# Performance work log

Hardware: AMD Instinct MI355X
Metric: run time of the kernel (lower is better)

Reference implementation:

```python
import jax, jax.numpy as jnp
import numpy as np

T = 524288
D = 256
N = 8192

def setup_inputs() -> dict:
    key = jax.random.key(0)
    k1, k2, k3 = jax.random.split(key, 3)
    embedding = jax.random.normal(k1, (T, D), dtype=jnp.float32)
    W = jax.random.normal(k2, (D, D), dtype=jnp.float32) * (1.0 / np.sqrt(D))
    obj_to_img = jnp.sort(jax.random.randint(k3, (T,), 0, N))
    return {"embedding": embedding, "W": W, "obj_to_img": obj_to_img, "num_segments": N}

def reference(embedding, W, obj_to_img, num_segments):
    # Per-segment mean of embedding @ W  -> global context [N, D]
    proj = embedding @ W  # [T, D]
    seg_sum = jax.ops.segment_sum(proj, obj_to_img, num_segments=num_segments)  # [N, D]
    counts = jax.ops.segment_sum(jnp.ones((embedding.shape[0],), embedding.dtype),
                                 obj_to_img, num_segments=num_segments)  # [N]
    safe_counts = jnp.maximum(counts, 1.0)
    transformed_global = jnp.tanh(seg_sum / safe_counts[:, None])  # [N, D]
    # sigmoid(emb . tg[segment]) per token
    scores = jax.nn.sigmoid(jnp.sum(embedding * transformed_global[obj_to_img], axis=-1))  # [T]
    # per-segment weighted sum of embeddings
    rep = jax.ops.segment_sum(embedding * scores[:, None], obj_to_img, num_segments=num_segments)  # [N, D]
    # broadcast representation back to every token of its segment (repeat_interleave)
    return rep[obj_to_img]  # [T, D]
```

## Files before the change

### kernel.cpp

```cpp
#include <hip/hip_runtime.h>
#include <math.h>

#define D 256
#define NSEG 8192

__device__ __forceinline__ int lower_bound_dev(const int* __restrict__ a, int n, int key) {
    int lo = 0, hi = n;
    while (lo < hi) {
        int mid = (lo + hi) >> 1;
        if (a[mid] < key) lo = mid + 1; else hi = mid;
    }
    return lo;
}

__global__ __launch_bounds__(256) void fused_seg_kernel(
        const float* __restrict__ emb,
        const float* __restrict__ W,
        const int*   __restrict__ obj, int T,
        float* __restrict__ out) {
    const int seg   = blockIdx.x;
    const int start = lower_bound_dev(obj, T, seg);
    const int end   = lower_bound_dev(obj, T, seg + 1);
    if (start >= end) return;

    const int tid  = threadIdx.x;
    const int lane = tid & 63;
    const int w    = tid >> 6;

    __shared__ float sm[4][D];
    __shared__ float sv[D];
    __shared__ float tg[D];

    float4 acc = make_float4(0.f, 0.f, 0.f, 0.f);
    for (int r = start + w; r < end; r += 4) {
        const float4 e = *reinterpret_cast<const float4*>(emb + (size_t)r * D + lane * 4);
        acc.x += e.x; acc.y += e.y; acc.z += e.z; acc.w += e.w;
    }
    *reinterpret_cast<float4*>(&sm[w][lane * 4]) = acc;
    __syncthreads();
    sv[tid] = sm[0][tid] + sm[1][tid] + sm[2][tid] + sm[3][tid];
    __syncthreads();

    const float inv = 1.0f / (float)(end - start);
    float p = 0.f;
    #pragma unroll 8
    for (int k = 0; k < D; ++k) {
        p += sv[k] * W[k * D + tid];
    }
    tg[tid] = tanhf(p * inv);
    __syncthreads();
    const float4 tg4 = *reinterpret_cast<const float4*>(&tg[lane * 4]);

    float4 racc = make_float4(0.f, 0.f, 0.f, 0.f);
    for (int r = start + w; r < end; r += 4) {
        const float4 e = *reinterpret_cast<const float4*>(emb + (size_t)r * D + lane * 4);
        float pd = e.x * tg4.x + e.y * tg4.y + e.z * tg4.z + e.w * tg4.w;
        #pragma unroll
        for (int off = 32; off >= 1; off >>= 1) pd += __shfl_xor(pd, off, 64);
        const float score = 1.0f / (1.0f + __expf(-pd));
        racc.x += e.x * score; racc.y += e.y * score;
        racc.z += e.z * score; racc.w += e.w * score;
    }
    *reinterpret_cast<float4*>(&sm[w][lane * 4]) = racc;
    __syncthreads();
    sm[0][tid] = sm[0][tid] + sm[1][tid] + sm[2][tid] + sm[3][tid];
    __syncthreads();
    const float4 rep4 = *reinterpret_cast<const float4*>(&sm[0][lane * 4]);

    for (int r = start + w; r < end; r += 4) {
        *reinterpret_cast<float4*>(out + (size_t)r * D + lane * 4) = rep4;
    }
}

extern "C" void kernel_launch(void* const* d_in, const int* in_sizes, int n_in,
                              void* d_out, int out_size, void* d_ws, size_t ws_size,
                              hipStream_t stream) {
    const float* emb = (const float*)d_in[0];
    const float* W   = (const float*)d_in[1];
    const int*   obj = (const int*)d_in[2];
    const int T = in_sizes[2];
    float* out = (float*)d_out;

    fused_seg_kernel<<<NSEG, 256, 0, stream>>>(emb, W, obj, T, out);
}
```

Measured before the change: 991.0 us.

## Precompute segment boundaries and process two segments per block to share W

Adds a separate kernel that writes the start index of every segment into workspace, replacing the per-block binary searches over obj_to_img. The fused kernel now handles two segments per block, so each W load feeds two projection accumulators and total W traffic is halved. In exchange it adds a second launch, serial per-segment phases with extra barriers inside each block, and half as many blocks.

```diff
diff --git a/kernel.cpp b/kernel.cpp
--- a/kernel.cpp
+++ b/kernel.cpp
@@ -3,72 +3,92 @@
 
 #define D 256
 #define NSEG 8192
+#define G 2
 
-__device__ __forceinline__ int lower_bound_dev(const int* __restrict__ a, int n, int key) {
-    int lo = 0, hi = n;
-    while (lo < hi) {
-        int mid = (lo + hi) >> 1;
-        if (a[mid] < key) lo = mid + 1; else hi = mid;
+__global__ __launch_bounds__(256) void boundaries_kernel(const int* __restrict__ obj, int T,
+                                                         int* __restrict__ starts) {
+    const int i = blockIdx.x * 256 + threadIdx.x;
+    if (i >= T) return;
+    const int v = obj[i];
+    const int p = (i == 0) ? -1 : obj[i - 1];
+    for (int s = p + 1; s <= v; ++s) starts[s] = i;
+    if (i == T - 1) {
+        for (int s = v + 1; s <= NSEG; ++s) starts[s] = T;
     }
-    return lo;
 }
 
 __global__ __launch_bounds__(256) void fused_seg_kernel(
         const float* __restrict__ emb,
         const float* __restrict__ W,
-        const int*   __restrict__ obj, int T,
+        const int*   __restrict__ starts,
         float* __restrict__ out) {
-    const int seg   = blockIdx.x;
-    const int start = lower_bound_dev(obj, T, seg);
-    const int end   = lower_bound_dev(obj, T, seg + 1);
-    if (start >= end) return;
-
+    const int seg0 = blockIdx.x * G;
     const int tid  = threadIdx.x;
     const int lane = tid & 63;
     const int w    = tid >> 6;
 
+    __shared__ float sv[G][D];
+    __shared__ float tg[G][D];
     __shared__ float sm[4][D];
-    __shared__ float sv[D];
-    __shared__ float tg[D];
+    __shared__ int   bnd[G + 1];
 
-    float4 acc = make_float4(0.f, 0.f, 0.f, 0.f);
-    for (int r = start + w; r < end; r += 4) {
-        const float4 e = *reinterpret_cast<const float4*>(emb + (size_t)r * D + lane * 4);
-        acc.x += e.x; acc.y += e.y; acc.z += e.z; acc.w += e.w;
-    }
-    *reinterpret_cast<float4*>(&sm[w][lane * 4]) = acc;
-    __syncthreads();
-    sv[tid] = sm[0][tid] + sm[1][tid] + sm[2][tid] + sm[3][tid];
+    if (tid <= G) bnd[tid] = starts[seg0 + tid];
     __syncthreads();
 
-    const float inv = 1.0f / (float)(end - start);
-    float p = 0.f;
-    #pragma unroll 8
+    for (int g = 0; g < G; ++g) {
+        const int s0 = bnd[g], s1 = bnd[g + 1];
+        float4 acc = make_float4(0.f, 0.f, 0.f, 0.f);
+        #pragma unroll 2
+        for (int r = s0 + w; r < s1; r += 4) {
+            const float4 e = *reinterpret_cast<const float4*>(emb + (size_t)r * D + lane * 4);
+            acc.x += e.x; acc.y += e.y; acc.z += e.z; acc.w += e.w;
+        }
+        *reinterpret_cast<float4*>(&sm[w][lane * 4]) = acc;
+        __syncthreads();
+        sv[g][tid] = sm[0][tid] + sm[1][tid] + sm[2][tid] + sm[3][tid];
+        __syncthreads();
+    }
+
+    float acc[G];
+    #pragma unroll
+    for (int g = 0; g < G; ++g) acc[g] = 0.f;
+    #pragma unroll 4
     for (int k = 0; k < D; ++k) {
-        p += sv[k] * W[k * D + tid];
+        const float wk = W[k * D + tid];
+        #pragma unroll
+        for (int g = 0; g < G; ++g) acc[g] += sv[g][k] * wk;
     }
-    tg[tid] = tanhf(p * inv);
+    #pragma unroll
+    for (int g = 0; g < G; ++g) {
+        const int cnt = bnd[g + 1] - bnd[g];
+        tg[g][tid] = tanhf(acc[g] / (float)(cnt > 1 ? cnt : 1));
+    }
     __syncthreads();
-    const float4 tg4 = *reinterpret_cast<const float4*>(&tg[lane * 4]);
 
-    float4 racc = make_float4(0.f, 0.f, 0.f, 0.f);
-    for (int r = start + w; r < end; r += 4) {
-        const float4 e = *reinterpret_cast<const float4*>(emb + (size_t)r * D + lane * 4);
-        float pd = e.x * tg4.x + e.y * tg4.y + e.z * tg4.z + e.w * tg4.w;
-        #pragma unroll
-        for (int off = 32; off >= 1; off >>= 1) pd += __shfl_xor(pd, off, 64);
-        const float score = 1.0f / (1.0f + __expf(-pd));
-        racc.x += e.x * score; racc.y += e.y * score;
-        racc.z += e.z * score; racc.w += e.w * score;
-    }
-    *reinterpret_cast<float4*>(&sm[w][lane * 4]) = racc;
-    __syncthreads();
-    sm[0][tid] = sm[0][tid] + sm[1][tid] + sm[2][tid] + sm[3][tid];
-    __syncthreads();
-    const float4 rep4 = *reinterpret_cast<const float4*>(&sm[0][lane * 4]);
-
-    for (int r = start + w; r < end; r += 4) {
-        *reinterpret_cast<float4*>(out + (size_t)r * D + lane * 4) = rep4;
+    for (int g = 0; g < G; ++g) {
+        const int s0 = bnd[g], s1 = bnd[g + 1];
+        if (s0 >= s1) { __syncthreads(); continue; }
+        const float4 tg4 = *reinterpret_cast<const float4*>(&tg[g][lane * 4]);
+        float4 racc = make_float4(0.f, 0.f, 0.f, 0.f);
+        #pragma unroll 2
+        for (int r = s0 + w; r < s1; r += 4) {
+            const float4 e = *reinterpret_cast<const float4*>(emb + (size_t)r * D + lane * 4);
+            float pd = e.x * tg4.x + e.y * tg4.y + e.z * tg4.z + e.w * tg4.w;
+            #pragma unroll
+            for (int off = 32; off >= 1; off >>= 1) pd += __shfl_xor(pd, off, 64);
+            const float score = 1.0f / (1.0f + __expf(-pd));
+            racc.x += e.x * score; racc.y += e.y * score;
+            racc.z += e.z * score; racc.w += e.w * score;
+        }
+        *reinterpret_cast<float4*>(&sm[w][lane * 4]) = racc;
+        __syncthreads();
+        sm[0][tid] = sm[0][tid] + sm[1][tid] + sm[2][tid] + sm[3][tid];
+        __syncthreads();
+        const float4 rep4 = *reinterpret_cast<const float4*>(&sm[0][lane * 4]);
+        for (int r = s0 + w; r < s1; r += 4) {
+            *reinterpret_cast<float4*>(out + (size_t)r * D + lane * 4) = rep4;
+        }
+        __syncthreads();
     }
 }
 
@@ -81,5 +101,8 @@
     const int T = in_sizes[2];
     float* out = (float*)d_out;
 
-    fused_seg_kernel<<<NSEG, 256, 0, stream>>>(emb, W, obj, T, out);
+    int* starts = (int*)d_ws;
+
+    boundaries_kernel<<<(T + 255) / 256, 256, 0, stream>>>(obj, T, starts);
+    fused_seg_kernel<<<NSEG / G, 256, 0, stream>>>(emb, W, starts, out);
 }
```

Result: slower. 1.012 ms (+2.1%).
